# Optimization experiments

Hardware: AMD Instinct MI355X
Metric: run time of the kernel (lower is better)

Reference implementation:

```python
import jax, jax.numpy as jnp
import numpy as np

B, T, D, H, V = 4096, 193, 50, 50, 11


def setup_inputs() -> dict:
    key = jax.random.key(0)
    ks = jax.random.split(key, 7)
    s = 1.0 / np.sqrt(H)
    return {
        "x": jax.random.normal(ks[0], (B, T, D), dtype=jnp.float32),
        "W_ih": jax.random.uniform(ks[1], (4 * H, D), jnp.float32, -s, s),
        "W_hh": jax.random.uniform(ks[2], (4 * H, H), jnp.float32, -s, s),
        "b_ih": jax.random.uniform(ks[3], (4 * H,), jnp.float32, -s, s),
        "b_hh": jax.random.uniform(ks[4], (4 * H,), jnp.float32, -s, s),
        "fc_w": jax.random.uniform(ks[5], (V, H), jnp.float32, -s, s),
        "fc_b": jax.random.uniform(ks[6], (V,), jnp.float32, -s, s),
    }


def _lstm_last_h(x, W_ih, W_hh, b_ih, b_hh):
    # Precompute input projections for all timesteps: [T, B, 4H]
    xp = jnp.einsum("btd,gd->tbg", x, W_ih) + (b_ih + b_hh)
    h0 = jnp.zeros((x.shape[0], H), x.dtype)
    c0 = jnp.zeros((x.shape[0], H), x.dtype)

    def step(carry, xt):
        h, c = carry
        gates = xt + h @ W_hh.T  # [B, 4H]
        i, f, g, o = jnp.split(gates, 4, axis=-1)  # PyTorch gate order i,f,g,o
        i = jax.nn.sigmoid(i)
        f = jax.nn.sigmoid(f)
        g = jnp.tanh(g)
        o = jax.nn.sigmoid(o)
        c = f * c + i * g
        h = o * jnp.tanh(c)
        return (h, c), None

    (h_last, _), _ = jax.lax.scan(step, (h0, c0), xp)
    return h_last


def reference(x, W_ih, W_hh, b_ih, b_hh, fc_w, fc_b):
    h = _lstm_last_h(x, W_ih, W_hh, b_ih, b_hh)  # [B, H]
    logits = jax.nn.relu(h) @ fc_w.T + fc_b       # [B, V]
    return jax.nn.log_softmax(logits, axis=-1)
```

## Files before the change

### kernel.cpp

```cpp
#include <hip/hip_runtime.h>
#include <math.h>

#define B_   4096
#define T_   193
#define D_   50
#define H_   50
#define V_   11
#define BT   16
#define NBLK (B_ / BT)
#define CH   32
#define NCH  ((T_ + CH - 1) / CH)
#define NTHREADS 1024

typedef __bf16 bf16x8 __attribute__((ext_vector_type(8)));
typedef float  f32x4  __attribute__((ext_vector_type(4)));

__device__ __forceinline__ float sigf(float v) { return 1.0f / (1.0f + __expf(-v)); }
__device__ __forceinline__ float thf(float v)  { return 2.0f / (1.0f + __expf(-2.0f * v)) - 1.0f; }

__device__ __forceinline__ void lgkm_barrier() {
    asm volatile("s_waitcnt lgkmcnt(0)\n\ts_barrier" ::: "memory");
}

__global__ __launch_bounds__(NTHREADS) void lstm_mfma_kernel(
    const float* __restrict__ x,
    const float* __restrict__ W_ih,
    const float* __restrict__ W_hh,
    const float* __restrict__ b_ih,
    const float* __restrict__ b_hh,
    const float* __restrict__ fc_w,
    const float* __restrict__ fc_b,
    float* __restrict__ out)
{
    __shared__ __align__(16) unsigned short xs[2 * CH * 2 * 64 * 8];
    __shared__ __align__(16) unsigned short hb[2 * 2 * 64 * 8];
    __shared__ float hfin[BT * 53];
    __shared__ float lgts[BT][V_];

    const int tid  = threadIdx.x;
    const int wid  = tid >> 6;
    const int lane = tid & 63;
    const int n    = lane & 15;
    const int kg   = lane >> 4;
    const int row0 = blockIdx.x * BT;
    const bool active = (wid < 13);
    const int  tile   = wid;

    if (tid < 256) {
        int4 z; z.x = 0; z.y = 0; z.z = 0; z.w = 0;
        reinterpret_cast<int4*>(hb)[tid] = z;
    }
    if (tid < 32) {
        hb[((tid >> 4) * 2 + 1) * 512 + (48 + (tid & 15)) * 8 + 7] = 0x3F80;
    }

    bf16x8 wf[4];
    {
        #pragma unroll
        for (int s = 0; s < 4; ++s) {
            float tv[8];
            #pragma unroll
            for (int j = 0; j < 8; ++j) tv[j] = 0.0f;
            if (active) {
                const int gp = 16 * tile + n;
                const int q  = gp & 3;
                const int ju = gp >> 2;
                if (ju < 50) {
                    const int row = q * 50 + ju;
                    #pragma unroll
                    for (int j = 0; j < 8; ++j) {
                        const int k = s * 32 + kg * 8 + j;
                        float v = 0.0f;
                        if (k < 50)                  v = W_ih[row * 50 + k];
                        else if (k >= 64 && k < 114) v = W_hh[row * 50 + (k - 64)];
                        else if (k == 127)           v = b_ih[row] + b_hh[row];
                        tv[j] = v;
                    }
                }
            }
            bf16x8 w;
            #pragma unroll
            for (int j = 0; j < 8; ++j) w[j] = (__bf16)tv[j];
            wf[s] = w;
        }
    }

    const int u_   = 4 * tile + kg;
    const int hoff = (u_ >> 5) * 512 + ((((u_ & 31) >> 3) << 4) | n) * 8 + (u_ & 7);

    float2 P[4][4];

    auto loadChunk = [&](int c) {
        const int t0 = c * CH;
        const int L  = (T_ - t0 < CH) ? (T_ - t0) : CH;
        const int nfrag = L * 128;
        #pragma unroll
        for (int i = 0; i < 4; ++i) {
            const int fi = tid + i * NTHREADS;
            if (fi < nfrag) {
                const int tc  = fi >> 7;
                const int rem = fi & 127;
                const int s   = rem >> 6;
                const int l   = rem & 63;
                const int nn  = l & 15;
                const int kk  = l >> 4;
                const float* base = x + ((size_t)(row0 + nn) * T_ + (t0 + tc)) * D_;
                #pragma unroll
                for (int j = 0; j < 4; ++j) {
                    int col = 32 * s + kk * 8 + 2 * j;
                    if (col > 48) col = 48;
                    P[i][j] = *reinterpret_cast<const float2*>(base + col);
                }
            }
        }
    };
    auto writeChunk = [&](int c, int b) {
        const int t0 = c * CH;
        const int L  = (T_ - t0 < CH) ? (T_ - t0) : CH;
        const int nfrag = L * 128;
        #pragma unroll
        for (int i = 0; i < 4; ++i) {
            const int fi = tid + i * NTHREADS;
            if (fi < nfrag) {
                bf16x8 w;
                #pragma unroll
                for (int j = 0; j < 4; ++j) {
                    w[2 * j]     = (__bf16)P[i][j].x;
                    w[2 * j + 1] = (__bf16)P[i][j].y;
                }
                reinterpret_cast<int4*>(xs)[b * (CH * 128) + fi] =
                    __builtin_bit_cast(int4, w);
            }
        }
    };

    loadChunk(0);
    writeChunk(0, 0);
    __syncthreads();
    loadChunk(1);

    float cst = 0.0f;
    int cur = 0;
    const int4* xsv = reinterpret_cast<const int4*>(xs);

    for (int c = 0; c < NCH; ++c) {
        const int t0 = c * CH;
        const int L  = (T_ - t0 < CH) ? (T_ - t0) : CH;
        const int b  = c & 1;
        bf16x8 bx0 = __builtin_bit_cast(bf16x8, xsv[b * (CH * 128) + lane]);
        bf16x8 bx1 = __builtin_bit_cast(bf16x8, xsv[b * (CH * 128) + 64 + lane]);

        for (int tc = 0; tc < L; ++tc) {
            const bool last = (t0 + tc == T_ - 1);

            f32x4 acc;
            if (active) {
                const int4* hbv = reinterpret_cast<const int4*>(hb) + cur * 128;
                const bf16x8 bh0 = __builtin_bit_cast(bf16x8, hbv[lane]);
                const bf16x8 bh1 = __builtin_bit_cast(bf16x8, hbv[64 + lane]);
                f32x4 ax = {0.0f, 0.0f, 0.0f, 0.0f};
                ax = __builtin_amdgcn_mfma_f32_16x16x32_bf16(wf[0], bx0, ax, 0, 0, 0);
                ax = __builtin_amdgcn_mfma_f32_16x16x32_bf16(wf[1], bx1, ax, 0, 0, 0);
                f32x4 ah = {0.0f, 0.0f, 0.0f, 0.0f};
                ah = __builtin_amdgcn_mfma_f32_16x16x32_bf16(wf[2], bh0, ah, 0, 0, 0);
                ah = __builtin_amdgcn_mfma_f32_16x16x32_bf16(wf[3], bh1, ah, 0, 0, 0);
                acc = ax + ah;
            }

            const int tn = (tc + 1 < L) ? (tc + 1) : tc;
            const bf16x8 nx0 = __builtin_bit_cast(
                bf16x8, xsv[b * (CH * 128) + tn * 128 + lane]);
            const bf16x8 nx1 = __builtin_bit_cast(
                bf16x8, xsv[b * (CH * 128) + tn * 128 + 64 + lane]);

            if (active) {
                const float ii = sigf(acc[0]);
                const float ff = sigf(acc[1]);
                const float g2 = thf(acc[2]);
                const float oo = sigf(acc[3]);
                cst = ff * cst + ii * g2;
                const float h = oo * thf(cst);
                hb[(cur ^ 1) * 1024 + hoff] =
                    __builtin_bit_cast(unsigned short, (__bf16)h);
                if (last) hfin[n * 53 + u_] = h;
            }

            if (tc == L - 1) {
                if (c + 1 < NCH) writeChunk(c + 1, b ^ 1);
                if (c + 2 < NCH) loadChunk(c + 2);
            }

            lgkm_barrier();
            bx0 = nx0;
            bx1 = nx1;
            cur ^= 1;
        }
    }

    if (tid < BT * V_) {
        const int bn = tid / V_;
        const int v  = tid % V_;
        float a = fc_b[v];
        #pragma unroll
        for (int j = 0; j < 50; ++j) {
            float hj = hfin[bn * 53 + j];
            hj = hj > 0.0f ? hj : 0.0f;
            a = fmaf(hj, fc_w[v * 50 + j], a);
        }
        lgts[bn][v] = a;
    }
    __syncthreads();
    if (tid < BT * V_) {
        const int bn = tid / V_;
        const int v  = tid % V_;
        float m = -1e30f;
        #pragma unroll
        for (int u = 0; u < V_; ++u) m = fmaxf(m, lgts[bn][u]);
        float s = 0.0f;
        #pragma unroll
        for (int u = 0; u < V_; ++u) s += __expf(lgts[bn][u] - m);
        out[(size_t)(row0 + bn) * V_ + v] = lgts[bn][v] - m - __logf(s);
    }
}

extern "C" void kernel_launch(void* const* d_in, const int* in_sizes, int n_in,
                              void* d_out, int out_size, void* d_ws, size_t ws_size,
                              hipStream_t stream) {
    const float* x    = (const float*)d_in[0];
    const float* W_ih = (const float*)d_in[1];
    const float* W_hh = (const float*)d_in[2];
    const float* b_ih = (const float*)d_in[3];
    const float* b_hh = (const float*)d_in[4];
    const float* fc_w = (const float*)d_in[5];
    const float* fc_b = (const float*)d_in[6];
    float* out = (float*)d_out;

    lstm_mfma_kernel<<<NBLK, NTHREADS, 0, stream>>>(
        x, W_ih, W_hh, b_ih, b_hh, fc_w, fc_b, out);
}
```

Before: 188.6 us.

## Trim block to 13 active waves and precompute next-step input MFMA off critical path

Cuts the block from 16 waves to 13, dropping the 3 idle waves that only helped with chunk staging and barriers, so every wave does LSTM work. The input-projection MFMAs for step t+1 now run after the gate math of step t and seed the accumulator for the recurrent MFMAs. This shortens the serial dependency chain per timestep and removes the acc add. The final hidden state is written to shared memory once after the loop instead of behind a per-step branch. Chunk loading now needs 5 passes per thread instead of 4, which raises register pressure.

After: 180.2 us, median of 2. 4.5% less time.

```diff
diff --git a/kernel.cpp b/kernel.cpp
--- a/kernel.cpp
+++ b/kernel.cpp
@@ -10,7 +10,8 @@
 #define NBLK (B_ / BT)
 #define CH   32
 #define NCH  ((T_ + CH - 1) / CH)
-#define NTHREADS 1024
+#define NTHREADS 832
+#define NP   ((CH * 128 + NTHREADS - 1) / NTHREADS)
 
 typedef __bf16 bf16x8 __attribute__((ext_vector_type(8)));
 typedef float  f32x4  __attribute__((ext_vector_type(4)));
@@ -43,8 +44,7 @@
     const int n    = lane & 15;
     const int kg   = lane >> 4;
     const int row0 = blockIdx.x * BT;
-    const bool active = (wid < 13);
-    const int  tile   = wid;
+    const int tile = wid;
 
     if (tid < 256) {
         int4 z; z.x = 0; z.y = 0; z.z = 0; z.w = 0;
@@ -61,21 +61,19 @@
             float tv[8];
             #pragma unroll
             for (int j = 0; j < 8; ++j) tv[j] = 0.0f;
-            if (active) {
-                const int gp = 16 * tile + n;
-                const int q  = gp & 3;
-                const int ju = gp >> 2;
-                if (ju < 50) {
-                    const int row = q * 50 + ju;
-                    #pragma unroll
-                    for (int j = 0; j < 8; ++j) {
-                        const int k = s * 32 + kg * 8 + j;
-                        float v = 0.0f;
-                        if (k < 50)                  v = W_ih[row * 50 + k];
-                        else if (k >= 64 && k < 114) v = W_hh[row * 50 + (k - 64)];
-                        else if (k == 127)           v = b_ih[row] + b_hh[row];
-                        tv[j] = v;
-                    }
+            const int gp = 16 * tile + n;
+            const int q  = gp & 3;
+            const int ju = gp >> 2;
+            if (ju < 50) {
+                const int row = q * 50 + ju;
+                #pragma unroll
+                for (int j = 0; j < 8; ++j) {
+                    const int k = s * 32 + kg * 8 + j;
+                    float v = 0.0f;
+                    if (k < 50)                  v = W_ih[row * 50 + k];
+                    else if (k >= 64 && k < 114) v = W_hh[row * 50 + (k - 64)];
+                    else if (k == 127)           v = b_ih[row] + b_hh[row];
+                    tv[j] = v;
                 }
             }
             bf16x8 w;
@@ -88,14 +86,14 @@
     const int u_   = 4 * tile + kg;
     const int hoff = (u_ >> 5) * 512 + ((((u_ & 31) >> 3) << 4) | n) * 8 + (u_ & 7);
 
-    float2 P[4][4];
+    float2 P[NP][4];
 
     auto loadChunk = [&](int c) {
         const int t0 = c * CH;
         const int L  = (T_ - t0 < CH) ? (T_ - t0) : CH;
         const int nfrag = L * 128;
         #pragma unroll
-        for (int i = 0; i < 4; ++i) {
+        for (int i = 0; i < NP; ++i) {
             const int fi = tid + i * NTHREADS;
             if (fi < nfrag) {
                 const int tc  = fi >> 7;
@@ -119,7 +117,7 @@
         const int L  = (T_ - t0 < CH) ? (T_ - t0) : CH;
         const int nfrag = L * 128;
         #pragma unroll
-        for (int i = 0; i < 4; ++i) {
+        for (int i = 0; i < NP; ++i) {
             const int fi = tid + i * NTHREADS;
             if (fi < nfrag) {
                 bf16x8 w;
@@ -140,6 +138,7 @@
     loadChunk(1);
 
     float cst = 0.0f;
+    float hlast = 0.0f;
     int cur = 0;
     const int4* xsv = reinterpret_cast<const int4*>(xs);
 
@@ -147,42 +146,41 @@
         const int t0 = c * CH;
         const int L  = (T_ - t0 < CH) ? (T_ - t0) : CH;
         const int b  = c & 1;
-        bf16x8 bx0 = __builtin_bit_cast(bf16x8, xsv[b * (CH * 128) + lane]);
-        bf16x8 bx1 = __builtin_bit_cast(bf16x8, xsv[b * (CH * 128) + 64 + lane]);
+
+        f32x4 ax;
+        {
+            const bf16x8 bx0 = __builtin_bit_cast(bf16x8, xsv[b * (CH * 128) + lane]);
+            const bf16x8 bx1 = __builtin_bit_cast(bf16x8, xsv[b * (CH * 128) + 64 + lane]);
+            f32x4 z = {0.0f, 0.0f, 0.0f, 0.0f};
+            z  = __builtin_amdgcn_mfma_f32_16x16x32_bf16(wf[0], bx0, z, 0, 0, 0);
+            ax = __builtin_amdgcn_mfma_f32_16x16x32_bf16(wf[1], bx1, z, 0, 0, 0);
+        }
 
         for (int tc = 0; tc < L; ++tc) {
-            const bool last = (t0 + tc == T_ - 1);
-
-            f32x4 acc;
-            if (active) {
-                const int4* hbv = reinterpret_cast<const int4*>(hb) + cur * 128;
-                const bf16x8 bh0 = __builtin_bit_cast(bf16x8, hbv[lane]);
-                const bf16x8 bh1 = __builtin_bit_cast(bf16x8, hbv[64 + lane]);
-                f32x4 ax = {0.0f, 0.0f, 0.0f, 0.0f};
-                ax = __builtin_amdgcn_mfma_f32_16x16x32_bf16(wf[0], bx0, ax, 0, 0, 0);
-                ax = __builtin_amdgcn_mfma_f32_16x16x32_bf16(wf[1], bx1, ax, 0, 0, 0);
-                f32x4 ah = {0.0f, 0.0f, 0.0f, 0.0f};
-                ah = __builtin_amdgcn_mfma_f32_16x16x32_bf16(wf[2], bh0, ah, 0, 0, 0);
-                ah = __builtin_amdgcn_mfma_f32_16x16x32_bf16(wf[3], bh1, ah, 0, 0, 0);
-                acc = ax + ah;
-            }
-
-            const int tn = (tc + 1 < L) ? (tc + 1) : tc;
-            const bf16x8 nx0 = __builtin_bit_cast(
-                bf16x8, xsv[b * (CH * 128) + tn * 128 + lane]);
-            const bf16x8 nx1 = __builtin_bit_cast(
-                bf16x8, xsv[b * (CH * 128) + tn * 128 + 64 + lane]);
-
-            if (active) {
-                const float ii = sigf(acc[0]);
-                const float ff = sigf(acc[1]);
-                const float g2 = thf(acc[2]);
-                const float oo = sigf(acc[3]);
-                cst = ff * cst + ii * g2;
-                const float h = oo * thf(cst);
-                hb[(cur ^ 1) * 1024 + hoff] =
-                    __builtin_bit_cast(unsigned short, (__bf16)h);
-                if (last) hfin[n * 53 + u_] = h;
+            const int4* hbv = reinterpret_cast<const int4*>(hb) + cur * 128;
+            const bf16x8 bh0 = __builtin_bit_cast(bf16x8, hbv[lane]);
+            const bf16x8 bh1 = __builtin_bit_cast(bf16x8, hbv[64 + lane]);
+            f32x4 a = __builtin_amdgcn_mfma_f32_16x16x32_bf16(wf[2], bh0, ax, 0, 0, 0);
+            a = __builtin_amdgcn_mfma_f32_16x16x32_bf16(wf[3], bh1, a, 0, 0, 0);
+
+            const float ii = sigf(a[0]);
+            const float ff = sigf(a[1]);
+            const float g2 = thf(a[2]);
+            const float oo = sigf(a[3]);
+            cst = ff * cst + ii * g2;
+            const float h = oo * thf(cst);
+            hlast = h;
+            hb[(cur ^ 1) * 1024 + hoff] =
+                __builtin_bit_cast(unsigned short, (__bf16)h);
+
+            if (tc + 1 < L) {
+                const bf16x8 nx0 = __builtin_bit_cast(
+                    bf16x8, xsv[b * (CH * 128) + (tc + 1) * 128 + lane]);
+                const bf16x8 nx1 = __builtin_bit_cast(
+                    bf16x8, xsv[b * (CH * 128) + (tc + 1) * 128 + 64 + lane]);
+                f32x4 z = {0.0f, 0.0f, 0.0f, 0.0f};
+                z  = __builtin_amdgcn_mfma_f32_16x16x32_bf16(wf[0], nx0, z, 0, 0, 0);
+                ax = __builtin_amdgcn_mfma_f32_16x16x32_bf16(wf[1], nx1, z, 0, 0, 0);
             }
 
             if (tc == L - 1) {
@@ -191,11 +189,12 @@
             }
 
             lgkm_barrier();
-            bx0 = nx0;
-            bx1 = nx1;
             cur ^= 1;
         }
     }
+
+    hfin[n * 53 + u_] = hlast;
+    __syncthreads();
 
     if (tid < BT * V_) {
         const int bn = tid / V_;
```
